# Performance work log

Hardware: AMD Instinct MI355X
Metric: run time of the kernel (lower is better)

The kernel has to match this reference:

```python
import jax, jax.numpy as jnp
import numpy as np

B, L, Q = 1024, 200, 1
DQ, DF = 512, 128
H, D1, D2 = 4, 128, 64


def setup_inputs() -> dict:
    key = jax.random.key(0)
    ks = jax.random.split(key, 20)
    inp = {
        "query": jax.random.normal(ks[0], (B, Q, DQ), jnp.float32),
        "fact": jax.random.normal(ks[1], (B, L, DF), jnp.float32),
        "mask": jax.random.randint(ks[2], (B, L), 0, 2, jnp.int32),
        "mm_cosine": jax.random.normal(ks[3], (2, B, L), jnp.float32),
    }
    # per-head FCRepeat weights, init per reset_parameters: randn/sqrt(fan_in), bias 0.1
    def w(k, fan_in, fan_out):
        return jax.random.normal(k, (H, fan_in, fan_out), jnp.float32) / np.sqrt(fan_in).astype(np.float32)
    inp["Wq1"] = w(ks[4], DQ, D1); inp["bq1"] = jnp.full((H, D1), 0.1, jnp.float32)
    inp["Wq2"] = w(ks[5], D1, D2); inp["bq2"] = jnp.full((H, D2), 0.1, jnp.float32)
    inp["Wf1"] = w(ks[6], DF, D1); inp["bf1"] = jnp.full((H, D1), 0.1, jnp.float32)
    inp["Wf2"] = w(ks[7], D1, D2); inp["bf2"] = jnp.full((H, D2), 0.1, jnp.float32)
    inp["Wv1"] = w(ks[8], DF, D1); inp["bv1"] = jnp.full((H, D1), 0.1, jnp.float32)
    inp["Wv2"] = w(ks[9], D1, D2); inp["bv2"] = jnp.full((H, D2), 0.1, jnp.float32)
    inp["tau1"] = jnp.full((2, H), 0.1, jnp.float32)   # cosine_tau1
    inp["tau2"] = jnp.full((3, H), 1.0, jnp.float32)   # cosine_tau2
    return inp


def _silu(x):
    return x * jax.nn.sigmoid(x)


def reference(query, fact, mask, mm_cosine,
              Wq1, bq1, Wq2, bq2, Wf1, bf1, Wf2, bf2, Wv1, bv1, Wv2, bv2,
              tau1, tau2):
    # per-head FC stacks (identity acts inside FCRepeat), then SiLU gating
    fq = jnp.einsum('bqi,hio->hbqo', query, Wq1) + bq1[:, None, None, :]
    fq = jnp.einsum('hbqi,hio->hbqo', fq, Wq2) + bq2[:, None, None, :]
    fq = _silu(fq)                                   # [H,B,1,D2]
    ff = jnp.einsum('bli,hio->hblo', fact, Wf1) + bf1[:, None, None, :]
    ff = jnp.einsum('hbli,hio->hblo', ff, Wf2) + bf2[:, None, None, :]
    ff = _silu(ff)                                   # [H,B,L,D2]
    fv = jnp.einsum('bli,hio->hblo', fact, Wv1) + bv1[:, None, None, :]
    fv = jnp.einsum('hbli,hio->hblo', fv, Wv2) + bv2[:, None, None, :]
    fv = _silu(fv)                                   # [H,B,L,D2]

    dot = jnp.einsum('hbld,hbqd->hblq', ff, fq)      # [H,B,L,1]
    dot = dot + (-1e9) * (1.0 - mask.astype(jnp.float32))[None, :, :, None]

    # cosine-bias cross terms
    bias = (mm_cosine[0][None] / tau1[0][:, None, None]
            + mm_cosine[1][None] / tau1[1][:, None, None])[..., None]  # [H,B,L,1]
    b1, b2, b3 = (tau2[i][:, None, None, None] for i in range(3))
    dot = b1 * dot + b2 * bias + b3 * dot * bias

    alphas = jax.nn.softmax(dot, axis=2) + 1e-7      # softmax over L
    out = jnp.einsum('hbld,hblq->hbdq', fv, alphas)[..., 0]  # [H,B,D2]
    return jnp.transpose(out, (1, 0, 2)).reshape(out.shape[1], -1)  # [B,H*D2]
```

## Files before the change

kernel.cpp:

```cpp
#include <hip/hip_runtime.h>
#include <hip/hip_bf16.h>

typedef __attribute__((ext_vector_type(8))) short short8;
typedef __attribute__((ext_vector_type(4))) float f32x4;

#define NH   4
#define NB   1024
#define NL   200
#define NDQ  512
#define NDF  128
#define ND1  128
#define ND2  64
#define KP   128
#define NW   13
#define NT   (NW*64)
#define HIMG (3*ND2*KP*2)
#define SGRAN (3*ND2*16)

#define OFF_WQC   0
#define OFF_BQC   (NH*NDQ*ND2*4)
#define OFF_FQ    (OFF_BQC + NH*ND2*4)
#define OFF_WIMG  (OFF_FQ + NH*NB*ND2*4)
#define OFF_BFC   (OFF_WIMG + NH*HIMG)
#define OFF_BVC   (OFF_BFC + NH*ND2*4)

#define GLOAD_LDS16(gp, lp) __builtin_amdgcn_global_load_lds(                 \
    (const __attribute__((address_space(1))) void*)(gp),                      \
    (__attribute__((address_space(3))) void*)(lp), 16, 0, 0)

__device__ inline short f2bf(float f) {
    union { float f; unsigned u; } v; v.f = f;
    unsigned r = (v.u + 0x7FFFu + ((v.u >> 16) & 1u)) >> 16;
    return (short)r;
}
__device__ inline float bf2f(short s) {
    union { unsigned u; float f; } v; v.u = ((unsigned)(unsigned short)s) << 16;
    return v.f;
}
__device__ inline float fsilu(float z) {
    return z * __fdividef(1.f, 1.f + __expf(-z));
}

template<int CTRL>
__device__ inline float dppf(float x) {
    return __int_as_float(__builtin_amdgcn_update_dpp(0, __float_as_int(x), CTRL, 0xF, 0xF, true));
}
__device__ inline float red16_add(float s) {
    s += dppf<0xB1>(s);
    s += dppf<0x4E>(s);
    s += dppf<0x141>(s);
    s += dppf<0x140>(s);
    return s;
}
__device__ inline float swap16_add(float x) {
    auto p = __builtin_amdgcn_permlane16_swap(__float_as_uint(x), __float_as_uint(x), false, false);
    return __uint_as_float(p[0]) + __uint_as_float(p[1]);
}
__device__ inline float swap32_add(float x) {
    auto p = __builtin_amdgcn_permlane32_swap(__float_as_uint(x), __float_as_uint(x), false, false);
    return __uint_as_float(p[0]) + __uint_as_float(p[1]);
}
__device__ inline float swap16_max(float x) {
    auto p = __builtin_amdgcn_permlane16_swap(__float_as_uint(x), __float_as_uint(x), false, false);
    return fmaxf(__uint_as_float(p[0]), __uint_as_float(p[1]));
}
__device__ inline float swap32_max(float x) {
    auto p = __builtin_amdgcn_permlane32_swap(__float_as_uint(x), __float_as_uint(x), false, false);
    return fmaxf(__uint_as_float(p[0]), __uint_as_float(p[1]));
}

__global__ __launch_bounds__(256) void k_combine(
    const float* __restrict__ Wq1, const float* __restrict__ bq1,
    const float* __restrict__ Wq2, const float* __restrict__ bq2,
    const float* __restrict__ Wf1, const float* __restrict__ bf1,
    const float* __restrict__ Wf2, const float* __restrict__ bf2,
    const float* __restrict__ Wv1, const float* __restrict__ bv1,
    const float* __restrict__ Wv2, const float* __restrict__ bv2,
    float* __restrict__ WQC, float* __restrict__ BQC,
    __hip_bfloat16* __restrict__ WIMG, float* __restrict__ BFC, float* __restrict__ BVC)
{
    int g = blockIdx.x * 256 + threadIdx.x;
    if (g < NH*NDQ*ND2) {
        int h = g >> 15, r = g & 32767, i = r >> 6, j = r & 63;
        const float* a  = Wq1 + (h*NDQ + i)*ND1;
        const float* bb = Wq2 + h*ND1*ND2 + j;
        float s = 0.f;
        for (int k = 0; k < ND1; ++k) s += a[k] * bb[k*ND2];
        WQC[(h*NDQ + i)*ND2 + j] = s;
        return;
    }
    g -= NH*NDQ*ND2;
    if (g < 2*NH*NDF*ND2) {
        int which = (g >= NH*NDF*ND2);
        int r0 = g & (NH*NDF*ND2 - 1);
        int h = r0 >> 13, r = r0 & 8191, i = r >> 6, j = r & 63;
        const float* W1 = (which ? Wv1 : Wf1) + (h*NDF + i)*ND1;
        const float* W2 = (which ? Wv2 : Wf2) + h*ND1*ND2 + j;
        float s = 0.f;
        for (int k = 0; k < ND1; ++k) s += W1[k] * W2[k*ND2];
        short hi = f2bf(s);
        short lo = f2bf(s - bf2f(hi));
        __hip_bfloat16* img = WIMG + (size_t)((h*3 + (which ? 2 : 0))*ND2 + j)*KP + i;
        ((short*)img)[0] = hi;
        if (!which) ((short*)img)[ND2*KP] = lo;
        return;
    }
    g -= 2*NH*NDF*ND2;
    if (g < NH*ND2) {
        int h = g >> 6, j = g & 63;
        float s = bq2[h*ND2 + j];
        for (int k = 0; k < ND1; ++k) s += bq1[h*ND1 + k] * Wq2[(h*ND1 + k)*ND2 + j];
        BQC[g] = s; return;
    }
    g -= NH*ND2;
    if (g < NH*ND2) {
        int h = g >> 6, j = g & 63;
        float s = bf2[h*ND2 + j];
        for (int k = 0; k < ND1; ++k) s += bf1[h*ND1 + k] * Wf2[(h*ND1 + k)*ND2 + j];
        BFC[g] = s; return;
    }
    g -= NH*ND2;
    if (g < NH*ND2) {
        int h = g >> 6, j = g & 63;
        float s = bv2[h*ND2 + j];
        for (int k = 0; k < ND1; ++k) s += bv1[h*ND1 + k] * Wv2[(h*ND1 + k)*ND2 + j];
        BVC[g] = s; return;
    }
}

__global__ __launch_bounds__(256) void k_fq(
    const float* __restrict__ query, const float* __restrict__ WQC,
    const float* __restrict__ BQC, float* __restrict__ FQ)
{
    __shared__ __align__(16) float qS[2*NDQ];
    const int t = threadIdx.x;
    const int b0 = blockIdx.x * 2;
    {
        const float4* src = (const float4*)(query + (size_t)b0 * NDQ);
        ((float4*)qS)[t] = src[t];
    }
    __syncthreads();
    const int h = t >> 6, d = t & 63;
    float s0, s1;
    s0 = s1 = BQC[h*ND2 + d];
    const float* wp = WQC + (size_t)h*NDQ*ND2 + d;
    #pragma unroll 16
    for (int i = 0; i < NDQ; ++i) {
        float wv = wp[i*ND2];
        s0 += qS[i]       * wv;
        s1 += qS[NDQ + i] * wv;
    }
    float* o = FQ + ((size_t)h*NB + b0)*ND2 + d;
    o[0]   = fsilu(s0);
    o[ND2] = fsilu(s1);
}

__global__ __launch_bounds__(NT) __attribute__((amdgpu_waves_per_eu(4, 4))) void k_main(
    const float* __restrict__ fact,
    const int* __restrict__ mask,
    const float* __restrict__ mmc,
    const float* __restrict__ tau1,
    const float* __restrict__ tau2,
    const float* __restrict__ FQ,
    const float* __restrict__ BFC,
    const float* __restrict__ BVC,
    const __hip_bfloat16* __restrict__ WIMG,
    float* __restrict__ out)
{
    __shared__ __align__(16) __hip_bfloat16 wS[2][3*ND2*KP];
    __shared__ __align__(16) float pS[2][NW][132];
    __shared__ __align__(16) float fqS[NH][ND2];
    __shared__ __align__(16) float bfcS[NH][ND2];
    __shared__ __align__(16) float bvcS[NH][ND2];

    const int t    = threadIdx.x;
    const int b    = blockIdx.x;
    const int w    = t >> 6;
    const int lane = t & 63;
    const int a15  = lane & 15;
    const int quad = lane >> 4;
    const int qrot = quad + 2*(a15 & 7);

    const int bL = b * NL;

    int srcOff[4], ldsByte[4];
    bool cOk[4];
    #pragma unroll
    for (int j = 0; j < 4; ++j) {
        int c = w*4 + j;
        cOk[j] = (c < SGRAN/64);
        int i = c*64 + lane;
        int row = i >> 4, gp = i & 15;
        int g = (gp - 2*(row & 7)) & 15;
        srcOff[j] = (row*16 + g) * 16;
        ldsByte[j] = c * 1024;
    }
    #pragma unroll
    for (int j = 0; j < 4; ++j)
        if (cOk[j])
            GLOAD_LDS16((const char*)WIMG + srcOff[j], (char*)&wS[0][0] + ldsByte[j]);

    float cval = 0.f;
    if (t < 256)       cval = FQ[(((size_t)(t >> 6))*NB + b)*ND2 + (t & 63)];
    else if (t < 512)  cval = BFC[t - 256];
    else if (t < 768)  cval = BVC[t - 512];
    float mkv[4], c0v[4], c1v[4];
    {
        int rbase = w*16 + quad*4;
        for (int rg = 0; rg < 4; ++rg) {
            int r = rbase + rg;
            if (r < NL) {
                mkv[rg] = 1e9f * (1.0f - (float)mask[bL + r]);
                c0v[rg] = mmc[bL + r];
                c1v[rg] = mmc[NB*NL + bL + r];
            } else { mkv[rg] = 0.f; c0v[rg] = 0.f; c1v[rg] = 0.f; }
        }
    }

    short8 afh[4], afl[4];
    const short8 zero8 = {0,0,0,0,0,0,0,0};
    {
        int row = w*16 + a15;
        for (int kk = 0; kk < 4; ++kk) {
            short8 vh = zero8, vl = zero8;
            if (row < NL) {
                const float* p = fact + ((size_t)(bL + row))*NDF + kk*32 + quad*8;
                float4 x0 = *(const float4*)p;
                float4 x1 = *(const float4*)(p + 4);
                float v[8] = {x0.x, x0.y, x0.z, x0.w, x1.x, x1.y, x1.z, x1.w};
                for (int j = 0; j < 8; ++j) {
                    short hs = f2bf(v[j]);
                    vh[j] = hs;
                    vl[j] = f2bf(v[j] - bf2f(hs));
                }
            }
            afh[kk] = vh;
            afl[kk] = vl;
        }
    }

    if (t < 256)       ((float*)fqS)[t]        = cval;
    else if (t < 512)  ((float*)bfcS)[t - 256] = cval;
    else if (t < 768)  ((float*)bvcS)[t - 512] = cval;
    __syncthreads();

    const f32x4 zf = {0.f, 0.f, 0.f, 0.f};

    for (int h = 0; h < NH; ++h) {
        if (h + 1 < NH) {
            const char* hb = (const char*)WIMG + (size_t)(h+1)*HIMG;
            char* lb = (char*)&wS[(h+1) & 1][0];
            #pragma unroll
            for (int j = 0; j < 4; ++j)
                if (cOk[j]) GLOAD_LDS16(hb + srcOff[j], lb + ldsByte[j]);
        }
        if (h > 0 && w == 8 + h) {
            const int ps = (h - 1) & 1;
            float M = pS[ps][0][0];
            for (int ww = 1; ww < NW; ++ww) M = fmaxf(M, pS[ps][ww][0]);
            float den = 0.f, num = 0.f, s1 = 0.f;
            for (int ww = 0; ww < NW; ++ww) {
                float e = __expf(pS[ps][ww][0] - M);
                den += e * pS[ps][ww][1];
                num += e * pS[ps][ww][2 + lane];
                s1  += pS[ps][ww][66 + lane];
            }
            out[(size_t)b*(NH*ND2) + (h-1)*ND2 + lane] = num * __fdividef(1.f, den) + 1e-7f * s1;
        }

        const float rt1a = __fdividef(1.f, tau1[h]);
        const float rt1b = __fdividef(1.f, tau1[NH + h]);
        const float t20 = tau2[h];
        const float t21 = tau2[NH + h];
        const float t22 = tau2[2*NH + h];

        float fqv[4], bfcv[4];
        for (int nt = 0; nt < 4; ++nt) {
            fqv[nt]  = fqS[h][nt*16 + a15];
            bfcv[nt] = bfcS[h][nt*16 + a15];
        }

        const __hip_bfloat16* wb = &wS[h & 1][0];

        f32x4 acc[4];
        for (int nt = 0; nt < 4; ++nt) acc[nt] = zf;
        __builtin_amdgcn_s_setprio(1);
        for (int kk = 0; kk < 4; ++kk) {
            const int gk = ((kk*4 + qrot) & 15) << 3;
            short8 bh[4], bl[4];
            for (int nt = 0; nt < 4; ++nt) {
                const __hip_bfloat16* p = wb + (nt*16 + a15)*KP + gk;
                bh[nt] = *(const short8*)p;
                bl[nt] = *(const short8*)(p + ND2*KP);
            }
            for (int nt = 0; nt < 4; ++nt) {
                acc[nt] = __builtin_amdgcn_mfma_f32_16x16x32_bf16(afh[kk], bh[nt], acc[nt], 0, 0, 0);
                acc[nt] = __builtin_amdgcn_mfma_f32_16x16x32_bf16(afh[kk], bl[nt], acc[nt], 0, 0, 0);
                acc[nt] = __builtin_amdgcn_mfma_f32_16x16x32_bf16(afl[kk], bh[nt], acc[nt], 0, 0, 0);
            }
        }
        __builtin_amdgcn_s_setprio(0);

        float lg[4];
        for (int rg = 0; rg < 4; ++rg) {
            float l = -3.0e38f;
            float s = 0.f;
            for (int nt = 0; nt < 4; ++nt)
                s += fsilu(acc[nt][rg] + bfcv[nt]) * fqv[nt];
            s = red16_add(s);
            int r = w*16 + quad*4 + rg;
            if (r < NL) {
                float dv = s - mkv[rg];
                float bias = c0v[rg]*rt1a + c1v[rg]*rt1b;
                l = t20*dv + t21*bias + t22*dv*bias;
            }
            lg[rg] = l;
        }

        float m = fmaxf(fmaxf(lg[0], lg[1]), fmaxf(lg[2], lg[3]));
        m = swap32_max(swap16_max(m));
        float sw = 0.f;
        for (int rg = 0; rg < 4; ++rg) {
            float p = __expf(lg[rg] - m);
            lg[rg] = p;
            sw += p;
        }
        sw = swap32_add(swap16_add(sw));

        for (int nt = 0; nt < 4; ++nt) acc[nt] = zf;
        __builtin_amdgcn_s_setprio(1);
        for (int kk = 0; kk < 4; ++kk) {
            const int gk = ((kk*4 + qrot) & 15) << 3;
            short8 bv[4];
            for (int nt = 0; nt < 4; ++nt)
                bv[nt] = *(const short8*)(wb + (2*ND2 + nt*16 + a15)*KP + gk);
            for (int nt = 0; nt < 4; ++nt)
                acc[nt] = __builtin_amdgcn_mfma_f32_16x16x32_bf16(afh[kk], bv[nt], acc[nt], 0, 0, 0);
        }
        __builtin_amdgcn_s_setprio(0);

        float bvcv[4];
        for (int nt = 0; nt < 4; ++nt) bvcv[nt] = bvcS[h][nt*16 + a15];
        float oE[4] = {0.f,0.f,0.f,0.f}, oS[4] = {0.f,0.f,0.f,0.f};
        for (int rg = 0; rg < 4; ++rg) {
            float p = lg[rg];
            int r = w*16 + quad*4 + rg;
            float vm = (r < NL) ? 1.f : 0.f;
            for (int nt = 0; nt < 4; ++nt) {
                float sv = fsilu(acc[nt][rg] + bvcv[nt]);
                oE[nt] += p * sv;
                oS[nt] += vm * sv;
            }
        }
        for (int nt = 0; nt < 4; ++nt) {
            oE[nt] = swap32_add(swap16_add(oE[nt]));
            oS[nt] = swap32_add(swap16_add(oS[nt]));
        }
        if (lane == 0) { pS[h & 1][w][0] = m; pS[h & 1][w][1] = sw; }
        if (quad == 0)
            for (int nt = 0; nt < 4; ++nt) {
                pS[h & 1][w][2  + nt*16 + a15] = oE[nt];
                pS[h & 1][w][66 + nt*16 + a15] = oS[nt];
            }
        __syncthreads();
    }

    if (w == 12) {
        const int ps = (NH - 1) & 1;
        float M = pS[ps][0][0];
        for (int ww = 1; ww < NW; ++ww) M = fmaxf(M, pS[ps][ww][0]);
        float den = 0.f, num = 0.f, s1 = 0.f;
        for (int ww = 0; ww < NW; ++ww) {
            float e = __expf(pS[ps][ww][0] - M);
            den += e * pS[ps][ww][1];
            num += e * pS[ps][ww][2 + lane];
            s1  += pS[ps][ww][66 + lane];
        }
        out[(size_t)b*(NH*ND2) + (NH-1)*ND2 + lane] = num * __fdividef(1.f, den) + 1e-7f * s1;
    }
}

extern "C" void kernel_launch(void* const* d_in, const int* in_sizes, int n_in,
                              void* d_out, int out_size, void* d_ws, size_t ws_size,
                              hipStream_t stream) {
    const float* query = (const float*)d_in[0];
    const float* fact  = (const float*)d_in[1];
    const int*   maskp = (const int*)d_in[2];
    const float* mmc   = (const float*)d_in[3];
    const float* Wq1 = (const float*)d_in[4];
    const float* bq1 = (const float*)d_in[5];
    const float* Wq2 = (const float*)d_in[6];
    const float* bq2 = (const float*)d_in[7];
    const float* Wf1 = (const float*)d_in[8];
    const float* bf1 = (const float*)d_in[9];
    const float* Wf2 = (const float*)d_in[10];
    const float* bf2 = (const float*)d_in[11];
    const float* Wv1 = (const float*)d_in[12];
    const float* bv1 = (const float*)d_in[13];
    const float* Wv2 = (const float*)d_in[14];
    const float* bv2 = (const float*)d_in[15];
    const float* tau1 = (const float*)d_in[16];
    const float* tau2 = (const float*)d_in[17];

    char* ws = (char*)d_ws;
    float*          WQC  = (float*)(ws + OFF_WQC);
    float*          BQC  = (float*)(ws + OFF_BQC);
    float*          FQ   = (float*)(ws + OFF_FQ);
    __hip_bfloat16* WIMG = (__hip_bfloat16*)(ws + OFF_WIMG);
    float*          BFC  = (float*)(ws + OFF_BFC);
    float*          BVC  = (float*)(ws + OFF_BVC);

    k_combine<<<771, 256, 0, stream>>>(Wq1, bq1, Wq2, bq2, Wf1, bf1, Wf2, bf2,
                                       Wv1, bv1, Wv2, bv2, WQC, BQC, WIMG, BFC, BVC);
    k_fq<<<NB/2, 256, 0, stream>>>(query, WQC, BQC, FQ);
    k_main<<<NB, NT, 0, stream>>>(fact, maskp, mmc, tau1, tau2, FQ, BFC, BVC, WIMG,
                                  (float*)d_out);
}
```

Baseline: 334.8 us.

## Fuse query projection into main kernel and split weight-combine reduction

Removes the separate k_fq launch. Each main-kernel block now computes its own query projection (query · WQC) with 768 threads splitting the 512-long reduction into three partial sums, then sums them in shared memory and applies SiLU. k_combine splits the Wq1·Wq2 product's K dimension across two thread halves, which doubles the block count and shortens serial loops. LDS offsets for the MFMA B-operand loads are precomputed into registers. This saves one launch and the FQ round trip through global memory. In exchange every main block reads the full 128KB WQC slice from cache, uses more registers and adds an extra barrier.

```diff
diff --git a/kernel.cpp b/kernel.cpp
--- a/kernel.cpp
+++ b/kernel.cpp
@@ -16,6 +16,7 @@
 #define NT   (NW*64)
 #define HIMG (3*ND2*KP*2)
 #define SGRAN (3*ND2*16)
+#define KC_GRID (1024 + 256 + 3)
 
 #define OFF_WQC   0
 #define OFF_BQC   (NH*NDQ*ND2*4)
@@ -79,24 +80,31 @@
     float* __restrict__ WQC, float* __restrict__ BQC,
     __hip_bfloat16* __restrict__ WIMG, float* __restrict__ BFC, float* __restrict__ BVC)
 {
-    int g = blockIdx.x * 256 + threadIdx.x;
-    if (g < NH*NDQ*ND2) {
-        int h = g >> 15, r = g & 32767, i = r >> 6, j = r & 63;
-        const float* a  = Wq1 + (h*NDQ + i)*ND1;
-        const float* bb = Wq2 + h*ND1*ND2 + j;
+    __shared__ float part[256];
+    const int blk = blockIdx.x, t = threadIdx.x;
+    if (blk < 1024) {
+        int o = blk*128 + (t & 127);
+        int kh = t >> 7;
+        int h = o >> 15, r = o & 32767, i = r >> 6, j = r & 63;
+        const float* a  = Wq1 + (h*NDQ + i)*ND1 + kh*64;
+        const float* bb = Wq2 + h*ND1*ND2 + kh*64*ND2 + j;
         float s = 0.f;
-        for (int k = 0; k < ND1; ++k) s += a[k] * bb[k*ND2];
-        WQC[(h*NDQ + i)*ND2 + j] = s;
+        #pragma unroll 16
+        for (int k = 0; k < 64; ++k) s += a[k] * bb[k*ND2];
+        part[t] = s;
+        __syncthreads();
+        if (t < 128) WQC[o] = part[t] + part[t + 128];
         return;
     }
-    g -= NH*NDQ*ND2;
-    if (g < 2*NH*NDF*ND2) {
+    if (blk < 1280) {
+        int g = (blk - 1024)*256 + t;
         int which = (g >= NH*NDF*ND2);
         int r0 = g & (NH*NDF*ND2 - 1);
         int h = r0 >> 13, r = r0 & 8191, i = r >> 6, j = r & 63;
         const float* W1 = (which ? Wv1 : Wf1) + (h*NDF + i)*ND1;
         const float* W2 = (which ? Wv2 : Wf2) + h*ND1*ND2 + j;
         float s = 0.f;
+        #pragma unroll 16
         for (int k = 0; k < ND1; ++k) s += W1[k] * W2[k*ND2];
         short hi = f2bf(s);
         short lo = f2bf(s - bf2f(hi));
@@ -105,54 +113,21 @@
         if (!which) ((short*)img)[ND2*KP] = lo;
         return;
     }
-    g -= 2*NH*NDF*ND2;
+    int g = (blk - 1280)*256 + t;
+    int h = (g >> 6) & 3, j = g & 63;
     if (g < NH*ND2) {
-        int h = g >> 6, j = g & 63;
         float s = bq2[h*ND2 + j];
         for (int k = 0; k < ND1; ++k) s += bq1[h*ND1 + k] * Wq2[(h*ND1 + k)*ND2 + j];
-        BQC[g] = s; return;
-    }
-    g -= NH*ND2;
-    if (g < NH*ND2) {
-        int h = g >> 6, j = g & 63;
+        BQC[g] = s;
+    } else if (g < 2*NH*ND2) {
         float s = bf2[h*ND2 + j];
         for (int k = 0; k < ND1; ++k) s += bf1[h*ND1 + k] * Wf2[(h*ND1 + k)*ND2 + j];
-        BFC[g] = s; return;
-    }
-    g -= NH*ND2;
-    if (g < NH*ND2) {
-        int h = g >> 6, j = g & 63;
+        BFC[h*ND2 + j] = s;
+    } else if (g < 3*NH*ND2) {
         float s = bv2[h*ND2 + j];
         for (int k = 0; k < ND1; ++k) s += bv1[h*ND1 + k] * Wv2[(h*ND1 + k)*ND2 + j];
-        BVC[g] = s; return;
-    }
-}
-
-__global__ __launch_bounds__(256) void k_fq(
-    const float* __restrict__ query, const float* __restrict__ WQC,
-    const float* __restrict__ BQC, float* __restrict__ FQ)
-{
-    __shared__ __align__(16) float qS[2*NDQ];
-    const int t = threadIdx.x;
-    const int b0 = blockIdx.x * 2;
-    {
-        const float4* src = (const float4*)(query + (size_t)b0 * NDQ);
-        ((float4*)qS)[t] = src[t];
-    }
-    __syncthreads();
-    const int h = t >> 6, d = t & 63;
-    float s0, s1;
-    s0 = s1 = BQC[h*ND2 + d];
-    const float* wp = WQC + (size_t)h*NDQ*ND2 + d;
-    #pragma unroll 16
-    for (int i = 0; i < NDQ; ++i) {
-        float wv = wp[i*ND2];
-        s0 += qS[i]       * wv;
-        s1 += qS[NDQ + i] * wv;
-    }
-    float* o = FQ + ((size_t)h*NB + b0)*ND2 + d;
-    o[0]   = fsilu(s0);
-    o[ND2] = fsilu(s1);
+        BVC[h*ND2 + j] = s;
+    }
 }
 
 __global__ __launch_bounds__(NT) __attribute__((amdgpu_waves_per_eu(4, 4))) void k_main(
@@ -161,7 +136,9 @@
     const float* __restrict__ mmc,
     const float* __restrict__ tau1,
     const float* __restrict__ tau2,
-    const float* __restrict__ FQ,
+    const float* __restrict__ query,
+    const float* __restrict__ WQC,
+    const float* __restrict__ BQC,
     const float* __restrict__ BFC,
     const float* __restrict__ BVC,
     const __hip_bfloat16* __restrict__ WIMG,
@@ -169,6 +146,7 @@
 {
     __shared__ __align__(16) __hip_bfloat16 wS[2][3*ND2*KP];
     __shared__ __align__(16) float pS[2][NW][132];
+    __shared__ __align__(16) float fqP[3][256];
     __shared__ __align__(16) float fqS[NH][ND2];
     __shared__ __align__(16) float bfcS[NH][ND2];
     __shared__ __align__(16) float bvcS[NH][ND2];
@@ -200,10 +178,16 @@
         if (cOk[j])
             GLOAD_LDS16((const char*)WIMG + srcOff[j], (char*)&wS[0][0] + ldsByte[j]);
 
-    float cval = 0.f;
-    if (t < 256)       cval = FQ[(((size_t)(t >> 6))*NB + b)*ND2 + (t & 63)];
-    else if (t < 512)  cval = BFC[t - 256];
-    else if (t < 768)  cval = BVC[t - 512];
+    int ldsOff[16];
+    #pragma unroll
+    for (int kk = 0; kk < 4; ++kk)
+        #pragma unroll
+        for (int nt = 0; nt < 4; ++nt)
+            ldsOff[kk*4 + nt] = (((nt*16 + a15)*KP) + (((kk*4 + qrot) & 15) << 3)) * 2;
+
+    float cv0 = 0.f;
+    if (t < 256)       cv0 = BFC[t];
+    else if (t < 512)  cv0 = BVC[t - 256];
     float mkv[4], c0v[4], c1v[4];
     {
         int rbase = w*16 + quad*4;
@@ -239,9 +223,25 @@
         }
     }
 
-    if (t < 256)       ((float*)fqS)[t]        = cval;
-    else if (t < 512)  ((float*)bfcS)[t - 256] = cval;
-    else if (t < 768)  ((float*)bvcS)[t - 512] = cval;
+    if (t < 256)       ((float*)bfcS)[t]       = cv0;
+    else if (t < 512)  ((float*)bvcS)[t - 256] = cv0;
+
+    if (t < 768) {
+        const int third = t >> 8;
+        const int o     = t & 255;
+        const int hq    = o >> 6, dq = o & 63;
+        const int i0    = third * 171;
+        const int len   = (third == 2) ? 170 : 171;
+        const float* qp = query + (size_t)b*NDQ + i0;
+        const float* wp = WQC + ((size_t)hq*NDQ + i0)*ND2 + dq;
+        float s = 0.f;
+        #pragma unroll 8
+        for (int i = 0; i < len; ++i) s += qp[i] * wp[i*ND2];
+        fqP[third][o] = s;
+    }
+    __syncthreads();
+    if (t < 256)
+        ((float*)fqS)[t] = fsilu(fqP[0][t] + fqP[1][t] + fqP[2][t] + BQC[t]);
     __syncthreads();
 
     const f32x4 zf = {0.f, 0.f, 0.f, 0.f};
@@ -280,18 +280,17 @@
             bfcv[nt] = bfcS[h][nt*16 + a15];
         }
 
-        const __hip_bfloat16* wb = &wS[h & 1][0];
+        const char* wbc = (const char*)&wS[h & 1][0];
 
         f32x4 acc[4];
         for (int nt = 0; nt < 4; ++nt) acc[nt] = zf;
         __builtin_amdgcn_s_setprio(1);
         for (int kk = 0; kk < 4; ++kk) {
-            const int gk = ((kk*4 + qrot) & 15) << 3;
             short8 bh[4], bl[4];
             for (int nt = 0; nt < 4; ++nt) {
-                const __hip_bfloat16* p = wb + (nt*16 + a15)*KP + gk;
+                const char* p = wbc + ldsOff[kk*4 + nt];
                 bh[nt] = *(const short8*)p;
-                bl[nt] = *(const short8*)(p + ND2*KP);
+                bl[nt] = *(const short8*)(p + 16384);
             }
             for (int nt = 0; nt < 4; ++nt) {
                 acc[nt] = __builtin_amdgcn_mfma_f32_16x16x32_bf16(afh[kk], bh[nt], acc[nt], 0, 0, 0);
@@ -330,10 +329,9 @@
         for (int nt = 0; nt < 4; ++nt) acc[nt] = zf;
         __builtin_amdgcn_s_setprio(1);
         for (int kk = 0; kk < 4; ++kk) {
-            const int gk = ((kk*4 + qrot) & 15) << 3;
             short8 bv[4];
             for (int nt = 0; nt < 4; ++nt)
-                bv[nt] = *(const short8*)(wb + (2*ND2 + nt*16 + a15)*KP + gk);
+                bv[nt] = *(const short8*)(wbc + ldsOff[kk*4 + nt] + 32768);
             for (int nt = 0; nt < 4; ++nt)
                 acc[nt] = __builtin_amdgcn_mfma_f32_16x16x32_bf16(afh[kk], bv[nt], acc[nt], 0, 0, 0);
         }
@@ -405,14 +403,12 @@
     char* ws = (char*)d_ws;
     float*          WQC  = (float*)(ws + OFF_WQC);
     float*          BQC  = (float*)(ws + OFF_BQC);
-    float*          FQ   = (float*)(ws + OFF_FQ);
     __hip_bfloat16* WIMG = (__hip_bfloat16*)(ws + OFF_WIMG);
     float*          BFC  = (float*)(ws + OFF_BFC);
     float*          BVC  = (float*)(ws + OFF_BVC);
 
-    k_combine<<<771, 256, 0, stream>>>(Wq1, bq1, Wq2, bq2, Wf1, bf1, Wf2, bf2,
-                                       Wv1, bv1, Wv2, bv2, WQC, BQC, WIMG, BFC, BVC);
-    k_fq<<<NB/2, 256, 0, stream>>>(query, WQC, BQC, FQ);
-    k_main<<<NB, NT, 0, stream>>>(fact, maskp, mmc, tau1, tau2, FQ, BFC, BVC, WIMG,
-                                  (float*)d_out);
-}
+    k_combine<<<KC_GRID, 256, 0, stream>>>(Wq1, bq1, Wq2, bq2, Wf1, bf1, Wf2, bf2,
+                                           Wv1, bv1, Wv2, bv2, WQC, BQC, WIMG, BFC, BVC);
+    k_main<<<NB, NT, 0, stream>>>(fact, maskp, mmc, tau1, tau2, query, WQC, BQC,
+                                  BFC, BVC, WIMG, (float*)d_out);
+}
```

New measurement: 354.3 us. +5.8%, slower.

## Software-pipeline head loop so next head's MFMAs overlap current head's softmax

Applied to the files above, without the earlier changes.

The per-head loop becomes an explicitly unrolled two-stage pipeline. Both the fact-path and value-path GEMMs for head h+1 are issued before the SiLU, softmax and partial-sum epilogue of head h runs, using two alternating accumulator sets. The aim is to let MFMA work hide the VALU and transcendental epilogue and to cut barrier-bound idle time. This holds more accumulators live, which raises register pressure, and it drops the s_setprio hints.

```diff
diff --git a/kernel.cpp b/kernel.cpp
--- a/kernel.cpp
+++ b/kernel.cpp
@@ -183,22 +183,22 @@
 
     const int bL = b * NL;
 
-    int srcOff[4], ldsByte[4];
-    bool cOk[4];
-    #pragma unroll
-    for (int j = 0; j < 4; ++j) {
-        int c = w*4 + j;
-        cOk[j] = (c < SGRAN/64);
-        int i = c*64 + lane;
-        int row = i >> 4, gp = i & 15;
-        int g = (gp - 2*(row & 7)) & 15;
-        srcOff[j] = (row*16 + g) * 16;
-        ldsByte[j] = c * 1024;
-    }
-    #pragma unroll
-    for (int j = 0; j < 4; ++j)
-        if (cOk[j])
-            GLOAD_LDS16((const char*)WIMG + srcOff[j], (char*)&wS[0][0] + ldsByte[j]);
+    auto DMA = [&](int hh) {
+        const char* hb = (const char*)WIMG + (size_t)hh*HIMG;
+        char* lb = (char*)&wS[hh & 1][0];
+        #pragma unroll
+        for (int j = 0; j < 4; ++j) {
+            int c = w*4 + j;
+            if (c < SGRAN/64) {
+                int i = c*64 + lane;
+                int row = i >> 4;
+                int g = ((i & 15) - 2*(row & 7)) & 15;
+                GLOAD_LDS16(hb + (row*16 + g)*16, lb + c*1024);
+            }
+        }
+    };
+
+    DMA(0);
 
     float cval = 0.f;
     if (t < 256)       cval = FQ[(((size_t)(t >> 6))*NB + b)*ND2 + (t & 63)];
@@ -246,67 +246,60 @@
 
     const f32x4 zf = {0.f, 0.f, 0.f, 0.f};
 
-    for (int h = 0; h < NH; ++h) {
-        if (h + 1 < NH) {
-            const char* hb = (const char*)WIMG + (size_t)(h+1)*HIMG;
-            char* lb = (char*)&wS[(h+1) & 1][0];
-            #pragma unroll
-            for (int j = 0; j < 4; ++j)
-                if (cOk[j]) GLOAD_LDS16(hb + srcOff[j], lb + ldsByte[j]);
-        }
-        if (h > 0 && w == 8 + h) {
-            const int ps = (h - 1) & 1;
-            float M = pS[ps][0][0];
-            for (int ww = 1; ww < NW; ++ww) M = fmaxf(M, pS[ps][ww][0]);
-            float den = 0.f, num = 0.f, s1 = 0.f;
-            for (int ww = 0; ww < NW; ++ww) {
-                float e = __expf(pS[ps][ww][0] - M);
-                den += e * pS[ps][ww][1];
-                num += e * pS[ps][ww][2 + lane];
-                s1  += pS[ps][ww][66 + lane];
-            }
-            out[(size_t)b*(NH*ND2) + (h-1)*ND2 + lane] = num * __fdividef(1.f, den) + 1e-7f * s1;
-        }
-
+    auto GEMMS = [&](f32x4 (&aF)[4], f32x4 (&aV)[4], const __hip_bfloat16* wb) {
+        #pragma unroll
+        for (int nt = 0; nt < 4; ++nt) { aF[nt] = zf; aV[nt] = zf; }
+        #pragma unroll
+        for (int kk = 0; kk < 4; ++kk) {
+            const int gk = ((kk*4 + qrot) & 15) << 3;
+            short8 bh[4], bl[4];
+            #pragma unroll
+            for (int nt = 0; nt < 4; ++nt) {
+                const __hip_bfloat16* p = wb + (nt*16 + a15)*KP + gk;
+                bh[nt] = *(const short8*)p;
+                bl[nt] = *(const short8*)(p + ND2*KP);
+            }
+            #pragma unroll
+            for (int nt = 0; nt < 4; ++nt) {
+                aF[nt] = __builtin_amdgcn_mfma_f32_16x16x32_bf16(afh[kk], bh[nt], aF[nt], 0, 0, 0);
+                aF[nt] = __builtin_amdgcn_mfma_f32_16x16x32_bf16(afh[kk], bl[nt], aF[nt], 0, 0, 0);
+                aF[nt] = __builtin_amdgcn_mfma_f32_16x16x32_bf16(afl[kk], bh[nt], aF[nt], 0, 0, 0);
+            }
+        }
+        #pragma unroll
+        for (int kk = 0; kk < 4; ++kk) {
+            const int gk = ((kk*4 + qrot) & 15) << 3;
+            short8 bv[4];
+            #pragma unroll
+            for (int nt = 0; nt < 4; ++nt)
+                bv[nt] = *(const short8*)(wb + (2*ND2 + nt*16 + a15)*KP + gk);
+            #pragma unroll
+            for (int nt = 0; nt < 4; ++nt)
+                aV[nt] = __builtin_amdgcn_mfma_f32_16x16x32_bf16(afh[kk], bv[nt], aV[nt], 0, 0, 0);
+        }
+    };
+
+    auto FINISH = [&](f32x4 (&aF)[4], f32x4 (&aV)[4], int h) {
         const float rt1a = __fdividef(1.f, tau1[h]);
         const float rt1b = __fdividef(1.f, tau1[NH + h]);
         const float t20 = tau2[h];
         const float t21 = tau2[NH + h];
         const float t22 = tau2[2*NH + h];
-
-        float fqv[4], bfcv[4];
+        float fqv[4], bfcv[4], bvcv[4];
+        #pragma unroll
         for (int nt = 0; nt < 4; ++nt) {
             fqv[nt]  = fqS[h][nt*16 + a15];
             bfcv[nt] = bfcS[h][nt*16 + a15];
-        }
-
-        const __hip_bfloat16* wb = &wS[h & 1][0];
-
-        f32x4 acc[4];
-        for (int nt = 0; nt < 4; ++nt) acc[nt] = zf;
-        __builtin_amdgcn_s_setprio(1);
-        for (int kk = 0; kk < 4; ++kk) {
-            const int gk = ((kk*4 + qrot) & 15) << 3;
-            short8 bh[4], bl[4];
-            for (int nt = 0; nt < 4; ++nt) {
-                const __hip_bfloat16* p = wb + (nt*16 + a15)*KP + gk;
-                bh[nt] = *(const short8*)p;
-                bl[nt] = *(const short8*)(p + ND2*KP);
-            }
-            for (int nt = 0; nt < 4; ++nt) {
-                acc[nt] = __builtin_amdgcn_mfma_f32_16x16x32_bf16(afh[kk], bh[nt], acc[nt], 0, 0, 0);
-                acc[nt] = __builtin_amdgcn_mfma_f32_16x16x32_bf16(afh[kk], bl[nt], acc[nt], 0, 0, 0);
-                acc[nt] = __builtin_amdgcn_mfma_f32_16x16x32_bf16(afl[kk], bh[nt], acc[nt], 0, 0, 0);
-            }
-        }
-        __builtin_amdgcn_s_setprio(0);
-
+            bvcv[nt] = bvcS[h][nt*16 + a15];
+        }
         float lg[4];
+        #pragma unroll
         for (int rg = 0; rg < 4; ++rg) {
             float l = -3.0e38f;
             float s = 0.f;
+            #pragma unroll
             for (int nt = 0; nt < 4; ++nt)
-                s += fsilu(acc[nt][rg] + bfcv[nt]) * fqv[nt];
+                s += fsilu(aF[nt][rg] + bfcv[nt]) * fqv[nt];
             s = red16_add(s);
             int r = w*16 + quad*4 + rg;
             if (r < NL) {
@@ -316,57 +309,45 @@
             }
             lg[rg] = l;
         }
-
         float m = fmaxf(fmaxf(lg[0], lg[1]), fmaxf(lg[2], lg[3]));
         m = swap32_max(swap16_max(m));
         float sw = 0.f;
+        #pragma unroll
         for (int rg = 0; rg < 4; ++rg) {
             float p = __expf(lg[rg] - m);
             lg[rg] = p;
             sw += p;
         }
         sw = swap32_add(swap16_add(sw));
-
-        for (int nt = 0; nt < 4; ++nt) acc[nt] = zf;
-        __builtin_amdgcn_s_setprio(1);
-        for (int kk = 0; kk < 4; ++kk) {
-            const int gk = ((kk*4 + qrot) & 15) << 3;
-            short8 bv[4];
-            for (int nt = 0; nt < 4; ++nt)
-                bv[nt] = *(const short8*)(wb + (2*ND2 + nt*16 + a15)*KP + gk);
-            for (int nt = 0; nt < 4; ++nt)
-                acc[nt] = __builtin_amdgcn_mfma_f32_16x16x32_bf16(afh[kk], bv[nt], acc[nt], 0, 0, 0);
-        }
-        __builtin_amdgcn_s_setprio(0);
-
-        float bvcv[4];
-        for (int nt = 0; nt < 4; ++nt) bvcv[nt] = bvcS[h][nt*16 + a15];
         float oE[4] = {0.f,0.f,0.f,0.f}, oS[4] = {0.f,0.f,0.f,0.f};
+        #pragma unroll
         for (int rg = 0; rg < 4; ++rg) {
             float p = lg[rg];
             int r = w*16 + quad*4 + rg;
             float vm = (r < NL) ? 1.f : 0.f;
+            #pragma unroll
             for (int nt = 0; nt < 4; ++nt) {
-                float sv = fsilu(acc[nt][rg] + bvcv[nt]);
+                float sv = fsilu(aV[nt][rg] + bvcv[nt]);
                 oE[nt] += p * sv;
                 oS[nt] += vm * sv;
             }
         }
+        #pragma unroll
         for (int nt = 0; nt < 4; ++nt) {
             oE[nt] = swap32_add(swap16_add(oE[nt]));
             oS[nt] = swap32_add(swap16_add(oS[nt]));
         }
         if (lane == 0) { pS[h & 1][w][0] = m; pS[h & 1][w][1] = sw; }
         if (quad == 0)
+            #pragma unroll
             for (int nt = 0; nt < 4; ++nt) {
                 pS[h & 1][w][2  + nt*16 + a15] = oE[nt];
                 pS[h & 1][w][66 + nt*16 + a15] = oS[nt];
             }
-        __syncthreads();
-    }
-
-    if (w == 12) {
-        const int ps = (NH - 1) & 1;
+    };
+
+    auto MERGE = [&](int hm) {
+        const int ps = hm & 1;
         float M = pS[ps][0][0];
         for (int ww = 1; ww < NW; ++ww) M = fmaxf(M, pS[ps][ww][0]);
         float den = 0.f, num = 0.f, s1 = 0.f;
@@ -376,8 +357,36 @@
             num += e * pS[ps][ww][2 + lane];
             s1  += pS[ps][ww][66 + lane];
         }
-        out[(size_t)b*(NH*ND2) + (NH-1)*ND2 + lane] = num * __fdividef(1.f, den) + 1e-7f * s1;
-    }
+        out[(size_t)b*(NH*ND2) + hm*ND2 + lane] = num * __fdividef(1.f, den) + 1e-7f * s1;
+    };
+
+    f32x4 aFA[4], aVA[4], aFB[4], aVB[4];
+
+    DMA(1);
+    GEMMS(aFA, aVA, &wS[0][0]);
+    __syncthreads();
+
+    DMA(2);
+    GEMMS(aFB, aVB, &wS[1][0]);
+    FINISH(aFA, aVA, 0);
+    __syncthreads();
+
+    DMA(3);
+    if (w == 9) MERGE(0);
+    GEMMS(aFA, aVA, &wS[0][0]);
+    FINISH(aFB, aVB, 1);
+    __syncthreads();
+
+    if (w == 10) MERGE(1);
+    GEMMS(aFB, aVB, &wS[1][0]);
+    FINISH(aFA, aVA, 2);
+    __syncthreads();
+
+    if (w == 11) MERGE(2);
+    FINISH(aFB, aVB, 3);
+    __syncthreads();
+
+    if (w == 12) MERGE(3);
 }
 
 extern "C" void kernel_launch(void* const* d_in, const int* in_sizes, int n_in,
```

Result: slower. 384.4 us (+14.8%).
